# Optimization experiments

Hardware: AMD Instinct MI355X
Metric: run time of the kernel (lower is better)

Reference implementation:

```python
import jax, jax.numpy as jnp
import numpy as np

EPS = 1e-12  # matches torch F.normalize default eps


def _l2_normalize(x, axis=-1):
    norm = jnp.sqrt(jnp.sum(x * x, axis=axis, keepdims=True))
    return x / jnp.maximum(norm, EPS)


def setup_inputs() -> dict:
    key = jax.random.key(0)
    k1, k2 = jax.random.split(key)
    B, D, P = 8192, 512, 32768
    z_context = jax.random.normal(k1, (B, D), dtype=jnp.float32)
    prototypes = jax.random.normal(k2, (P, D), dtype=jnp.float32) * 0.02
    return {"z_context": z_context, "prototypes": prototypes, "topk": 3}


def reference(z_context, prototypes, topk):
    # Cosine similarity: normalize queries and prototype bank, then GEMM.
    z_norm = _l2_normalize(z_context, axis=-1)          # [B, D]
    p_norm = _l2_normalize(prototypes, axis=-1)         # [P, D]
    sim = jnp.einsum('bd,pd->bp', z_norm, p_norm)       # [B, P]
    k = min(topk, prototypes.shape[0])
    topk_val, topk_idx = jax.lax.top_k(sim, k)          # [B, k] each
    return sim, topk_idx, topk_val
```

## Files before the change

### kernel.cpp

```cpp
#include <hip/hip_runtime.h>
#include <float.h>
#include <stdint.h>

#define D_DIM 512

typedef __attribute__((ext_vector_type(8))) short bf16x8;
typedef __attribute__((ext_vector_type(4))) float f32x4;

#define GLD_LDS16(g, l)                                              \
    __builtin_amdgcn_global_load_lds(                                \
        (const __attribute__((address_space(1))) void*)(g),          \
        (__attribute__((address_space(3))) void*)(l), 16, 0, 0)

__device__ __forceinline__ uint32_t pk_bf16(float a, float b) {
    uint32_t ua = __builtin_bit_cast(uint32_t, a) + 0x8000u;
    uint32_t ub = __builtin_bit_cast(uint32_t, b) + 0x8000u;
    return (ua >> 16) | (ub & 0xFFFF0000u);
}

__global__ __launch_bounds__(256) void convert_norm_kernel(
        const float* __restrict__ X, unsigned short* __restrict__ Xb,
        float* __restrict__ r, int R) {
    int row = blockIdx.x * 4 + (threadIdx.x >> 6);
    if (row >= R) return;
    int lane = threadIdx.x & 63;
    const float* x = X + (size_t)row * D_DIM + lane * 8;
    float4 f0 = *(const float4*)(x);
    float4 f1 = *(const float4*)(x + 4);
    float s = f0.x*f0.x + f0.y*f0.y + f0.z*f0.z + f0.w*f0.w
            + f1.x*f1.x + f1.y*f1.y + f1.z*f1.z + f1.w*f1.w;
#pragma unroll
    for (int off = 32; off; off >>= 1) s += __shfl_xor(s, off);
    float rv = 1.0f / fmaxf(sqrtf(s), 1e-12f);
    if (lane == 0) r[row] = rv;
    uint4 w;
    w.x = pk_bf16(f0.x * rv, f0.y * rv);
    w.y = pk_bf16(f0.z * rv, f0.w * rv);
    w.z = pk_bf16(f1.x * rv, f1.y * rv);
    w.w = pk_bf16(f1.z * rv, f1.w * rv);
    *(uint4*)(Xb + (size_t)row * D_DIM + lane * 8) = w;
}

template <bool FUSE>
__global__ __launch_bounds__(256) void gemm_lds_bf16(
        const unsigned short* __restrict__ Zb,
        const unsigned short* __restrict__ Pb,
        float* __restrict__ sim, uint2* __restrict__ part, int Pn) {
    __shared__ __align__(16) unsigned char SH[65536];
    uint4* S = (uint4*)SH;

    int bi = blockIdx.x;
    int mb, nb;
    if (gridDim.x == 16384) {
        int xcd = bi & 7;
        int r = bi >> 3;
        mb = xcd * 8 + (r & 7);
        nb = r >> 3;
    } else {
        nb = bi % (Pn / 128);
        mb = bi / (Pn / 128);
    }
    const int bm = mb * 128, bn = nb * 128;

    const int tid = threadIdx.x;
    const int lane = tid & 63;
    const int wid = tid >> 6;
    const int wr = wid >> 1, wc = wid & 1;
    const int ln15 = lane & 15, hi = lane >> 4;

    const unsigned short* gA[4];
    const unsigned short* gB[4];
    int ldsIdx[4];
#pragma unroll
    for (int q = 0; q < 4; ++q) {
        int flat = q * 256 + tid;
        int row = flat >> 3;
        int c = flat & 7;
        int cg = c ^ (row & 7);
        gA[q] = Zb + (size_t)(bm + row) * D_DIM + cg * 8;
        gB[q] = Pb + (size_t)(bn + row) * D_DIM + cg * 8;
        ldsIdx[q] = flat;
    }

    f32x4 acc[4][4] = {};

#pragma unroll
    for (int q = 0; q < 4; ++q) {
        GLD_LDS16(gA[q], &S[ldsIdx[q]]);
        GLD_LDS16(gB[q], &S[1024 + ldsIdx[q]]);
        gA[q] += 64;
        gB[q] += 64;
    }

    int cur = 0;
#pragma unroll 1
    for (int s8 = 0; s8 < 8; ++s8) {
        const int nxt = cur ^ 1;
        if (s8 < 7) {
#pragma unroll
            for (int q = 0; q < 4; ++q) {
                GLD_LDS16(gA[q], &S[nxt * 2048 + ldsIdx[q]]);
                GLD_LDS16(gB[q], &S[nxt * 2048 + 1024 + ldsIdx[q]]);
                gA[q] += 64;
                gB[q] += 64;
            }
            asm volatile("s_waitcnt vmcnt(8)" ::: "memory");
        } else {
            asm volatile("s_waitcnt vmcnt(0)" ::: "memory");
        }
        __builtin_amdgcn_s_barrier();
        __builtin_amdgcn_sched_barrier(0);

        const int sb = cur * 2048;
        __builtin_amdgcn_s_setprio(1);
#pragma unroll
        for (int kk = 0; kk < 2; ++kk) {
            bf16x8 av[4], bv[4];
            const int kch = kk * 4 + hi;
#pragma unroll
            for (int t = 0; t < 4; ++t) {
                int arow = wr * 64 + t * 16 + ln15;
                av[t] = __builtin_bit_cast(bf16x8,
                        S[sb + arow * 8 + (kch ^ (arow & 7))]);
                int brow = wc * 64 + t * 16 + ln15;
                bv[t] = __builtin_bit_cast(bf16x8,
                        S[sb + 1024 + brow * 8 + (kch ^ (brow & 7))]);
            }
#pragma unroll
            for (int i = 0; i < 4; ++i)
#pragma unroll
                for (int j = 0; j < 4; ++j)
                    acc[i][j] = __builtin_amdgcn_mfma_f32_16x16x32_bf16(
                        av[i], bv[j], acc[i][j], 0, 0, 0);
        }
        __builtin_amdgcn_s_setprio(0);
        __builtin_amdgcn_sched_barrier(0);
        __builtin_amdgcn_s_barrier();
        cur = nxt;
    }

#pragma unroll
    for (int i = 0; i < 4; ++i) {
#pragma unroll
        for (int rr = 0; rr < 4; ++rr) {
            int row = bm + wr * 64 + i * 16 + hi * 4 + rr;
#pragma unroll
            for (int j = 0; j < 4; ++j) {
                int col = bn + wc * 64 + j * 16 + ln15;
                sim[(size_t)row * Pn + col] = acc[i][j][rr];
            }
        }
    }

    if constexpr (FUSE) {
        float* T = (float*)SH;
        uint2* M = (uint2*)(SH + 34816);
        const int NB = Pn >> 7;
        const int r = tid & 63;
        const int q = wid;
#pragma unroll 1
        for (int hf = 0; hf < 2; ++hf) {
            __syncthreads();
            if (wr == hf) {
#pragma unroll
                for (int i = 0; i < 4; ++i)
#pragma unroll
                    for (int j = 0; j < 4; ++j)
                        *(f32x4*)&T[(wc * 64 + j * 16 + ln15) * 68 + i * 16 + hi * 4]
                            = acc[i][j];
            }
            __syncthreads();
            float tv[4]; int ti[4];
#pragma unroll
            for (int k = 0; k < 4; ++k) { tv[k] = -FLT_MAX; ti[k] = 0x7FFFFFFF; }
#pragma unroll
            for (int c4 = 0; c4 < 32; c4 += 4) {
                float e0 = T[(q * 32 + c4 + 0) * 68 + r];
                float e1 = T[(q * 32 + c4 + 1) * 68 + r];
                float e2 = T[(q * 32 + c4 + 2) * 68 + r];
                float e3 = T[(q * 32 + c4 + 3) * 68 + r];
                float mg = fmaxf(fmaxf(e0, e1), fmaxf(e2, e3));
                if (mg > tv[3]) {
                    float ee[4] = {e0, e1, e2, e3};
#pragma unroll
                    for (int e = 0; e < 4; ++e) {
                        float val = ee[e];
                        if (val > tv[3]) {
                            int p = 3;
#pragma unroll
                            for (int j2 = 2; j2 >= 0; --j2)
                                if (val > tv[j2]) { tv[j2+1] = tv[j2]; ti[j2+1] = ti[j2]; p = j2; }
                            tv[p] = val; ti[p] = bn + q * 32 + c4 + e;
                        }
                    }
                }
            }
#pragma unroll
            for (int k = 0; k < 4; ++k)
                M[q * 256 + k * 64 + r] =
                    make_uint2(__builtin_bit_cast(uint32_t, tv[k]), (uint32_t)ti[k]);
            __syncthreads();
            if (tid < 64) {
                float fv[4]; int fi[4];
#pragma unroll
                for (int k = 0; k < 4; ++k) { fv[k] = -FLT_MAX; fi[k] = 0x7FFFFFFF; }
#pragma unroll
                for (int qq = 0; qq < 4; ++qq)
#pragma unroll
                    for (int k = 0; k < 4; ++k) {
                        uint2 u = M[qq * 256 + k * 64 + tid];
                        float val = __builtin_bit_cast(float, u.x);
                        if (val > fv[3]) {
                            int p = 3;
#pragma unroll
                            for (int j2 = 2; j2 >= 0; --j2)
                                if (val > fv[j2]) { fv[j2+1] = fv[j2]; fi[j2+1] = fi[j2]; p = j2; }
                            fv[p] = val; fi[p] = (int)u.y;
                        }
                    }
                size_t o = ((size_t)(bm + hf * 64 + tid) * NB + nb) * 4;
#pragma unroll
                for (int k = 0; k < 4; ++k)
                    part[o + k] =
                        make_uint2(__builtin_bit_cast(uint32_t, fv[k]), (uint32_t)fi[k]);
            }
        }
    }
}

__global__ __launch_bounds__(256) void topk_reduce(const uint2* __restrict__ part,
        const float* __restrict__ Z, const float* __restrict__ Pm,
        const float* __restrict__ rz, const float* __restrict__ rp,
        float* __restrict__ oidx, float* __restrict__ oval, int Pn) {
    int row = blockIdx.x * 4 + (threadIdx.x >> 6);
    int lane = threadIdx.x & 63;
    const int NB = Pn >> 7;
    const uint2* pr = part + (size_t)row * NB * 4;

    float v[8]; int ix[8];
#pragma unroll
    for (int j = 0; j < 8; ++j) { v[j] = -FLT_MAX; ix[j] = -1; }

    const int total = NB * 4;
    for (int c = lane; c < total; c += 64) {
        uint2 u = pr[c];
        float val = __builtin_bit_cast(float, u.x);
        if (val > v[7]) {
            int idx = (int)u.y;
            int pos = 7;
#pragma unroll
            for (int j = 6; j >= 0; --j) {
                if (val > v[j]) { v[j+1] = v[j]; ix[j+1] = ix[j]; pos = j; }
            }
            v[pos] = val; ix[pos] = idx;
        }
    }

    int cand[8];
#pragma unroll
    for (int k = 0; k < 8; ++k) {
        float bv = v[0]; int bi2 = ix[0];
#pragma unroll
        for (int off = 32; off; off >>= 1) {
            float ov = __shfl_xor(bv, off);
            int oi = __shfl_xor(bi2, off);
            if (ov > bv || (ov == bv && oi >= 0 && (unsigned)oi < (unsigned)bi2)) {
                bv = ov; bi2 = oi;
            }
        }
        cand[k] = bi2;
        if (bi2 == ix[0]) {
#pragma unroll
            for (int j = 0; j < 7; ++j) { v[j] = v[j+1]; ix[j] = ix[j+1]; }
            v[7] = -FLT_MAX; ix[7] = -1;
        }
    }

    float zv[8];
    const float* zrow = Z + (size_t)row * D_DIM + lane * 8;
#pragma unroll
    for (int j = 0; j < 8; ++j) zv[j] = zrow[j];
    float rzv = rz[row];

    float ex[8];
#pragma unroll
    for (int c = 0; c < 8; ++c) {
        int idx = cand[c];
        const float* prow = Pm + (size_t)idx * D_DIM + lane * 8;
        float s = 0.f;
#pragma unroll
        for (int j = 0; j < 8; ++j) s += zv[j] * prow[j];
#pragma unroll
        for (int off = 32; off; off >>= 1) s += __shfl_xor(s, off);
        ex[c] = s * rzv * rp[idx];
    }

    bool used[8] = {};
#pragma unroll
    for (int k = 0; k < 3; ++k) {
        float bv = -FLT_MAX; int bi2 = Pn; int bc = 0;
#pragma unroll
        for (int c = 0; c < 8; ++c) {
            if (!used[c] && (ex[c] > bv || (ex[c] == bv && cand[c] < bi2))) {
                bv = ex[c]; bi2 = cand[c]; bc = c;
            }
        }
        used[bc] = true;
        if (lane == 0) {
            oidx[(size_t)row * 3 + k] = (float)bi2;
            oval[(size_t)row * 3 + k] = bv;
        }
    }
}

__global__ __launch_bounds__(256) void rnorm_kernel(const float* __restrict__ X,
                                                    float* __restrict__ r, int R) {
    int row = blockIdx.x * 4 + (threadIdx.x >> 6);
    if (row >= R) return;
    int lane = threadIdx.x & 63;
    const float* x = X + (size_t)row * D_DIM;
    float s = 0.f;
#pragma unroll
    for (int t = 0; t < 2; ++t) {
        float4 v = *(const float4*)(x + (t * 64 + lane) * 4);
        s += v.x * v.x + v.y * v.y + v.z * v.z + v.w * v.w;
    }
#pragma unroll
    for (int off = 32; off; off >>= 1) s += __shfl_xor(s, off);
    if (lane == 0) r[row] = 1.0f / fmaxf(sqrtf(s), 1e-12f);
}

__global__ __launch_bounds__(256, 2) void gemm_bf16_sim(const float* __restrict__ Z,
        const float* __restrict__ Pm, const float* __restrict__ rz,
        const float* __restrict__ rp, float* __restrict__ sim, int Pn) {
    __shared__ uint4 As16[1024];
    __shared__ uint4 Bs16[1024];
    int bi = blockIdx.x;
    int mb, nb;
    if (gridDim.x == 16384) {
        int xcd = bi & 7;
        int r = bi >> 3;
        mb = xcd * 8 + (r & 7);
        nb = r >> 3;
    } else {
        nb = bi % (Pn / 128);
        mb = bi / (Pn / 128);
    }
    const int bm = mb * 128, bn = nb * 128;
    const int tid = threadIdx.x;
    const int srow = tid >> 1;
    const int half = tid & 1;
    const float* aP = Z  + (size_t)(bm + srow) * D_DIM + half * 32;
    const float* bP = Pm + (size_t)(bn + srow) * D_DIM + half * 32;
    const int lane = tid & 63;
    const int wid = tid >> 6;
    const int wr = wid >> 1, wc = wid & 1;
    const int ln15 = lane & 15, hi = lane >> 4;
    f32x4 acc[4][4] = {};
    float4 f[8], g[8];
#pragma unroll
    for (int q = 0; q < 8; ++q) {
        f[q] = *(const float4*)(aP + q * 4);
        g[q] = *(const float4*)(bP + q * 4);
    }
#pragma unroll 1
    for (int s = 0; s < 8; ++s) {
#pragma unroll
        for (int q8 = 0; q8 < 4; ++q8) {
            uint4 wa, wb;
            wa.x = pk_bf16(f[2*q8].x,   f[2*q8].y);
            wa.y = pk_bf16(f[2*q8].z,   f[2*q8].w);
            wa.z = pk_bf16(f[2*q8+1].x, f[2*q8+1].y);
            wa.w = pk_bf16(f[2*q8+1].z, f[2*q8+1].w);
            wb.x = pk_bf16(g[2*q8].x,   g[2*q8].y);
            wb.y = pk_bf16(g[2*q8].z,   g[2*q8].w);
            wb.z = pk_bf16(g[2*q8+1].x, g[2*q8+1].y);
            wb.w = pk_bf16(g[2*q8+1].z, g[2*q8+1].w);
            int colByte = half * 64 + q8 * 16;
            int idx = srow * 8 + ((colByte ^ ((srow & 7) << 4)) >> 4);
            As16[idx] = wa;
            Bs16[idx] = wb;
        }
        __syncthreads();
        if (s < 7) {
            int k0 = (s + 1) * 64;
#pragma unroll
            for (int q = 0; q < 8; ++q) {
                f[q] = *(const float4*)(aP + k0 + q * 4);
                g[q] = *(const float4*)(bP + k0 + q * 4);
            }
        }
#pragma unroll
        for (int kk = 0; kk < 2; ++kk) {
            bf16x8 av[4], bv[4];
            const int cb = kk * 64 + hi * 16;
#pragma unroll
            for (int t = 0; t < 4; ++t) {
                int arow = wr * 64 + t * 16 + ln15;
                av[t] = __builtin_bit_cast(bf16x8,
                        As16[arow * 8 + ((cb ^ ((arow & 7) << 4)) >> 4)]);
                int brow = wc * 64 + t * 16 + ln15;
                bv[t] = __builtin_bit_cast(bf16x8,
                        Bs16[brow * 8 + ((cb ^ ((brow & 7) << 4)) >> 4)]);
            }
#pragma unroll
            for (int i = 0; i < 4; ++i)
#pragma unroll
                for (int j = 0; j < 4; ++j)
                    acc[i][j] = __builtin_amdgcn_mfma_f32_16x16x32_bf16(
                        av[i], bv[j], acc[i][j], 0, 0, 0);
        }
        __syncthreads();
    }
    float rpv[4];
#pragma unroll
    for (int j = 0; j < 4; ++j) rpv[j] = rp[bn + wc * 64 + j * 16 + ln15];
#pragma unroll
    for (int i = 0; i < 4; ++i) {
#pragma unroll
        for (int rr = 0; rr < 4; ++rr) {
            int row = bm + wr * 64 + i * 16 + hi * 4 + rr;
            float rzv = rz[row];
#pragma unroll
            for (int j = 0; j < 4; ++j) {
                int col = bn + wc * 64 + j * 16 + ln15;
                sim[(size_t)row * Pn + col] = acc[i][j][rr] * rzv * rpv[j];
            }
        }
    }
}

__global__ __launch_bounds__(256) void topk_refine(const float* __restrict__ sim,
        const float* __restrict__ Z, const float* __restrict__ Pm,
        const float* __restrict__ rz, const float* __restrict__ rp,
        float* __restrict__ oidx, float* __restrict__ oval, int Pn) {
    int row = blockIdx.x * 4 + (threadIdx.x >> 6);
    int lane = threadIdx.x & 63;
    const float* rptr = sim + (size_t)row * Pn;

    float v[8]; int ix[8];
#pragma unroll
    for (int j = 0; j < 8; ++j) { v[j] = -FLT_MAX; ix[j] = -1; }

    const int iters = Pn >> 8;
    for (int t = 0; t < iters; ++t) {
        int base = t * 256 + lane * 4;
        float4 q = *(const float4*)(rptr + base);
        float vals[4] = {q.x, q.y, q.z, q.w};
#pragma unroll
        for (int e = 0; e < 4; ++e) {
            float val = vals[e];
            if (val > v[7]) {
                int idx = base + e;
                int pos = 7;
#pragma unroll
                for (int j = 6; j >= 0; --j) {
                    if (val > v[j]) { v[j+1] = v[j]; ix[j+1] = ix[j]; pos = j; }
                }
                v[pos] = val; ix[pos] = idx;
            }
        }
    }

    int cand[8];
#pragma unroll
    for (int k = 0; k < 8; ++k) {
        float bv = v[0]; int bi2 = ix[0];
#pragma unroll
        for (int off = 32; off; off >>= 1) {
            float ov = __shfl_xor(bv, off);
            int oi = __shfl_xor(bi2, off);
            if (ov > bv || (ov == bv && oi >= 0 && (unsigned)oi < (unsigned)bi2)) {
                bv = ov; bi2 = oi;
            }
        }
        cand[k] = bi2;
        if (bi2 == ix[0]) {
#pragma unroll
            for (int j = 0; j < 7; ++j) { v[j] = v[j+1]; ix[j] = ix[j+1]; }
            v[7] = -FLT_MAX; ix[7] = -1;
        }
    }

    float zv[8];
    const float* zrow = Z + (size_t)row * D_DIM + lane * 8;
#pragma unroll
    for (int j = 0; j < 8; ++j) zv[j] = zrow[j];
    float rzv = rz[row];

    float ex[8];
#pragma unroll
    for (int c = 0; c < 8; ++c) {
        int idx = cand[c];
        const float* prow = Pm + (size_t)idx * D_DIM + lane * 8;
        float s = 0.f;
#pragma unroll
        for (int j = 0; j < 8; ++j) s += zv[j] * prow[j];
#pragma unroll
        for (int off = 32; off; off >>= 1) s += __shfl_xor(s, off);
        ex[c] = s * rzv * rp[idx];
    }

    bool used[8] = {};
#pragma unroll
    for (int k = 0; k < 3; ++k) {
        float bv = -FLT_MAX; int bi2 = Pn; int bc = 0;
#pragma unroll
        for (int c = 0; c < 8; ++c) {
            if (!used[c] && (ex[c] > bv || (ex[c] == bv && cand[c] < bi2))) {
                bv = ex[c]; bi2 = cand[c]; bc = c;
            }
        }
        used[bc] = true;
        if (lane == 0) {
            oidx[(size_t)row * 3 + k] = (float)bi2;
            oval[(size_t)row * 3 + k] = bv;
        }
    }
}

extern "C" void kernel_launch(void* const* d_in, const int* in_sizes, int n_in,
                              void* d_out, int out_size, void* d_ws, size_t ws_size,
                              hipStream_t stream) {
    const float* Z  = (const float*)d_in[0];
    const float* Pm = (const float*)d_in[1];
    const int B  = in_sizes[0] / D_DIM;
    const int Pn = in_sizes[1] / D_DIM;

    float* sim  = (float*)d_out;
    float* oidx = sim + (size_t)B * Pn;
    float* oval = oidx + (size_t)B * 3;

    float* rz = (float*)d_ws;
    float* rp = rz + B;
    unsigned short* Zb = (unsigned short*)(rp + Pn);
    unsigned short* Pb = Zb + (size_t)B * D_DIM;
    uint2* part = (uint2*)(Pb + (size_t)Pn * D_DIM);

    const size_t NB = (size_t)Pn / 128;
    const size_t need_bf16  = (size_t)(B + Pn) * 4 + (size_t)(B + Pn) * D_DIM * 2;
    const size_t need_fused = need_bf16 + (size_t)B * NB * 4 * sizeof(uint2);

    dim3 grid((B / 128) * (Pn / 128));

    if (ws_size >= need_fused) {
        convert_norm_kernel<<<B / 4, 256, 0, stream>>>(Z, Zb, rz, B);
        convert_norm_kernel<<<Pn / 4, 256, 0, stream>>>(Pm, Pb, rp, Pn);
        gemm_lds_bf16<true><<<grid, 256, 0, stream>>>(Zb, Pb, sim, part, Pn);
        topk_reduce<<<B / 4, 256, 0, stream>>>(part, Z, Pm, rz, rp, oidx, oval, Pn);
    } else if (ws_size >= need_bf16) {
        convert_norm_kernel<<<B / 4, 256, 0, stream>>>(Z, Zb, rz, B);
        convert_norm_kernel<<<Pn / 4, 256, 0, stream>>>(Pm, Pb, rp, Pn);
        gemm_lds_bf16<false><<<grid, 256, 0, stream>>>(Zb, Pb, sim, nullptr, Pn);
        topk_refine<<<B / 4, 256, 0, stream>>>(sim, Z, Pm, rz, rp, oidx, oval, Pn);
    } else {
        rnorm_kernel<<<B / 4, 256, 0, stream>>>(Z, rz, B);
        rnorm_kernel<<<Pn / 4, 256, 0, stream>>>(Pm, rp, Pn);
        gemm_bf16_sim<<<grid, 256, 0, stream>>>(Z, Pm, rz, rp, sim, Pn);
        topk_refine<<<B / 4, 256, 0, stream>>>(sim, Z, Pm, rz, rp, oidx, oval, Pn);
    }
}
```

Measured before the change: 765.7 us.

## Halve GEMM K-tile to 32 and shrink LDS to 32KB for higher occupancy

```diff
diff --git a/kernel.cpp b/kernel.cpp
--- a/kernel.cpp
+++ b/kernel.cpp
@@ -42,11 +42,11 @@
 }
 
 template <bool FUSE>
-__global__ __launch_bounds__(256) void gemm_lds_bf16(
+__global__ __launch_bounds__(256, 4) void gemm_lds_bf16(
         const unsigned short* __restrict__ Zb,
         const unsigned short* __restrict__ Pb,
         float* __restrict__ sim, uint2* __restrict__ part, int Pn) {
-    __shared__ __align__(16) unsigned char SH[65536];
+    __shared__ __align__(16) unsigned char SH[32768];
     uint4* S = (uint4*)SH;
 
     int bi = blockIdx.x;
@@ -68,15 +68,15 @@
     const int wr = wid >> 1, wc = wid & 1;
     const int ln15 = lane & 15, hi = lane >> 4;
 
-    const unsigned short* gA[4];
-    const unsigned short* gB[4];
-    int ldsIdx[4];
-#pragma unroll
-    for (int q = 0; q < 4; ++q) {
+    const unsigned short* gA[2];
+    const unsigned short* gB[2];
+    int ldsIdx[2];
+#pragma unroll
+    for (int q = 0; q < 2; ++q) {
         int flat = q * 256 + tid;
-        int row = flat >> 3;
-        int c = flat & 7;
-        int cg = c ^ (row & 7);
+        int row = flat >> 2;
+        int c = flat & 3;
+        int cg = c ^ (row & 3);
         gA[q] = Zb + (size_t)(bm + row) * D_DIM + cg * 8;
         gB[q] = Pb + (size_t)(bn + row) * D_DIM + cg * 8;
         ldsIdx[q] = flat;
@@ -85,54 +85,50 @@
     f32x4 acc[4][4] = {};
 
 #pragma unroll
-    for (int q = 0; q < 4; ++q) {
+    for (int q = 0; q < 2; ++q) {
         GLD_LDS16(gA[q], &S[ldsIdx[q]]);
-        GLD_LDS16(gB[q], &S[1024 + ldsIdx[q]]);
-        gA[q] += 64;
-        gB[q] += 64;
+        GLD_LDS16(gB[q], &S[512 + ldsIdx[q]]);
+        gA[q] += 32;
+        gB[q] += 32;
     }
 
     int cur = 0;
 #pragma unroll 1
-    for (int s8 = 0; s8 < 8; ++s8) {
+    for (int s8 = 0; s8 < 16; ++s8) {
         const int nxt = cur ^ 1;
-        if (s8 < 7) {
-#pragma unroll
-            for (int q = 0; q < 4; ++q) {
-                GLD_LDS16(gA[q], &S[nxt * 2048 + ldsIdx[q]]);
-                GLD_LDS16(gB[q], &S[nxt * 2048 + 1024 + ldsIdx[q]]);
-                gA[q] += 64;
-                gB[q] += 64;
-            }
-            asm volatile("s_waitcnt vmcnt(8)" ::: "memory");
+        if (s8 < 15) {
+#pragma unroll
+            for (int q = 0; q < 2; ++q) {
+                GLD_LDS16(gA[q], &S[nxt * 1024 + ldsIdx[q]]);
+                GLD_LDS16(gB[q], &S[nxt * 1024 + 512 + ldsIdx[q]]);
+                gA[q] += 32;
+                gB[q] += 32;
+            }
+            asm volatile("s_waitcnt vmcnt(4)" ::: "memory");
         } else {
             asm volatile("s_waitcnt vmcnt(0)" ::: "memory");
         }
         __builtin_amdgcn_s_barrier();
         __builtin_amdgcn_sched_barrier(0);
 
-        const int sb = cur * 2048;
+        const int sb = cur * 1024;
         __builtin_amdgcn_s_setprio(1);
-#pragma unroll
-        for (int kk = 0; kk < 2; ++kk) {
-            bf16x8 av[4], bv[4];
-            const int kch = kk * 4 + hi;
-#pragma unroll
-            for (int t = 0; t < 4; ++t) {
-                int arow = wr * 64 + t * 16 + ln15;
-                av[t] = __builtin_bit_cast(bf16x8,
-                        S[sb + arow * 8 + (kch ^ (arow & 7))]);
-                int brow = wc * 64 + t * 16 + ln15;
-                bv[t] = __builtin_bit_cast(bf16x8,
-                        S[sb + 1024 + brow * 8 + (kch ^ (brow & 7))]);
-            }
-#pragma unroll
-            for (int i = 0; i < 4; ++i)
-#pragma unroll
-                for (int j = 0; j < 4; ++j)
-                    acc[i][j] = __builtin_amdgcn_mfma_f32_16x16x32_bf16(
-                        av[i], bv[j], acc[i][j], 0, 0, 0);
-        }
+        bf16x8 av[4], bv[4];
+#pragma unroll
+        for (int t = 0; t < 4; ++t) {
+            int arow = wr * 64 + t * 16 + ln15;
+            av[t] = __builtin_bit_cast(bf16x8,
+                    S[sb + arow * 4 + (hi ^ (arow & 3))]);
+            int brow = wc * 64 + t * 16 + ln15;
+            bv[t] = __builtin_bit_cast(bf16x8,
+                    S[sb + 512 + brow * 4 + (hi ^ (brow & 3))]);
+        }
+#pragma unroll
+        for (int i = 0; i < 4; ++i)
+#pragma unroll
+            for (int j = 0; j < 4; ++j)
+                acc[i][j] = __builtin_amdgcn_mfma_f32_16x16x32_bf16(
+                    av[i], bv[j], acc[i][j], 0, 0, 0);
         __builtin_amdgcn_s_setprio(0);
         __builtin_amdgcn_sched_barrier(0);
         __builtin_amdgcn_s_barrier();
@@ -154,75 +150,80 @@
 
     if constexpr (FUSE) {
         float* T = (float*)SH;
-        uint2* M = (uint2*)(SH + 34816);
+        uint2* M = (uint2*)(SH + 17408);
         const int NB = Pn >> 7;
         const int r = tid & 63;
-        const int q = wid;
+        const int q = tid >> 6;
 #pragma unroll 1
         for (int hf = 0; hf < 2; ++hf) {
-            __syncthreads();
-            if (wr == hf) {
-#pragma unroll
-                for (int i = 0; i < 4; ++i)
-#pragma unroll
-                    for (int j = 0; j < 4; ++j)
-                        *(f32x4*)&T[(wc * 64 + j * 16 + ln15) * 68 + i * 16 + hi * 4]
-                            = acc[i][j];
-            }
-            __syncthreads();
-            float tv[4]; int ti[4];
-#pragma unroll
-            for (int k = 0; k < 4; ++k) { tv[k] = -FLT_MAX; ti[k] = 0x7FFFFFFF; }
-#pragma unroll
-            for (int c4 = 0; c4 < 32; c4 += 4) {
-                float e0 = T[(q * 32 + c4 + 0) * 68 + r];
-                float e1 = T[(q * 32 + c4 + 1) * 68 + r];
-                float e2 = T[(q * 32 + c4 + 2) * 68 + r];
-                float e3 = T[(q * 32 + c4 + 3) * 68 + r];
-                float mg = fmaxf(fmaxf(e0, e1), fmaxf(e2, e3));
-                if (mg > tv[3]) {
-                    float ee[4] = {e0, e1, e2, e3};
-#pragma unroll
-                    for (int e = 0; e < 4; ++e) {
-                        float val = ee[e];
-                        if (val > tv[3]) {
-                            int p = 3;
-#pragma unroll
-                            for (int j2 = 2; j2 >= 0; --j2)
-                                if (val > tv[j2]) { tv[j2+1] = tv[j2]; ti[j2+1] = ti[j2]; p = j2; }
-                            tv[p] = val; ti[p] = bn + q * 32 + c4 + e;
+            float rv[4]; int ri[4];
+#pragma unroll
+            for (int k = 0; k < 4; ++k) { rv[k] = -FLT_MAX; ri[k] = 0x7FFFFFFF; }
+#pragma unroll 1
+            for (int ch = 0; ch < 2; ++ch) {
+                __syncthreads();
+                if (wr == hf && wc == ch) {
+#pragma unroll
+                    for (int i = 0; i < 4; ++i)
+#pragma unroll
+                        for (int j = 0; j < 4; ++j)
+                            *(f32x4*)&T[(j * 16 + ln15) * 68 + i * 16 + hi * 4]
+                                = acc[i][j];
+                }
+                __syncthreads();
+                float tv[4]; int ti[4];
+#pragma unroll
+                for (int k = 0; k < 4; ++k) { tv[k] = -FLT_MAX; ti[k] = 0x7FFFFFFF; }
+#pragma unroll
+                for (int c4 = 0; c4 < 16; c4 += 4) {
+                    float e0 = T[(q * 16 + c4 + 0) * 68 + r];
+                    float e1 = T[(q * 16 + c4 + 1) * 68 + r];
+                    float e2 = T[(q * 16 + c4 + 2) * 68 + r];
+                    float e3 = T[(q * 16 + c4 + 3) * 68 + r];
+                    float mg = fmaxf(fmaxf(e0, e1), fmaxf(e2, e3));
+                    if (mg > tv[3]) {
+                        float ee[4] = {e0, e1, e2, e3};
+#pragma unroll
+                        for (int e = 0; e < 4; ++e) {
+                            float val = ee[e];
+                            if (val > tv[3]) {
+                                int p = 3;
+#pragma unroll
+                                for (int j2 = 2; j2 >= 0; --j2)
+                                    if (val > tv[j2]) { tv[j2+1] = tv[j2]; ti[j2+1] = ti[j2]; p = j2; }
+                                tv[p] = val; ti[p] = bn + ch * 64 + q * 16 + c4 + e;
+                            }
                         }
                     }
                 }
-            }
-#pragma unroll
-            for (int k = 0; k < 4; ++k)
-                M[q * 256 + k * 64 + r] =
-                    make_uint2(__builtin_bit_cast(uint32_t, tv[k]), (uint32_t)ti[k]);
-            __syncthreads();
+#pragma unroll
+                for (int k = 0; k < 4; ++k)
+                    M[q * 256 + k * 64 + r] =
+                        make_uint2(__builtin_bit_cast(uint32_t, tv[k]), (uint32_t)ti[k]);
+                __syncthreads();
+                if (tid < 64) {
+#pragma unroll
+                    for (int qq = 0; qq < 4; ++qq)
+#pragma unroll
+                        for (int k = 0; k < 4; ++k) {
+                            uint2 u = M[qq * 256 + k * 64 + tid];
+                            float val = __builtin_bit_cast(float, u.x);
+                            if (val > rv[3]) {
+                                int p = 3;
+#pragma unroll
+                                for (int j2 = 2; j2 >= 0; --j2)
+                                    if (val > rv[j2]) { rv[j2+1] = rv[j2]; ri[j2+1] = ri[j2]; p = j2; }
+                                rv[p] = val; ri[p] = (int)u.y;
+                            }
+                        }
+                }
+            }
             if (tid < 64) {
-                float fv[4]; int fi[4];
-#pragma unroll
-                for (int k = 0; k < 4; ++k) { fv[k] = -FLT_MAX; fi[k] = 0x7FFFFFFF; }
-#pragma unroll
-                for (int qq = 0; qq < 4; ++qq)
-#pragma unroll
-                    for (int k = 0; k < 4; ++k) {
-                        uint2 u = M[qq * 256 + k * 64 + tid];
-                        float val = __builtin_bit_cast(float, u.x);
-                        if (val > fv[3]) {
-                            int p = 3;
-#pragma unroll
-                            for (int j2 = 2; j2 >= 0; --j2)
-                                if (val > fv[j2]) { fv[j2+1] = fv[j2]; fi[j2+1] = fi[j2]; p = j2; }
-                            fv[p] = val; fi[p] = (int)u.y;
-                        }
-                    }
                 size_t o = ((size_t)(bm + hf * 64 + tid) * NB + nb) * 4;
 #pragma unroll
                 for (int k = 0; k < 4; ++k)
                     part[o + k] =
-                        make_uint2(__builtin_bit_cast(uint32_t, fv[k]), (uint32_t)fi[k]);
+                        make_uint2(__builtin_bit_cast(uint32_t, rv[k]), (uint32_t)ri[k]);
             }
         }
     }
```

New measurement: 695.6 us. -9.2%, faster.
